# Kernel tuning notes

Measured on AMD Instinct MI355X. Metric: run time of the kernel, lower is better.

The kernel has to match this reference:

```python
import jax, jax.numpy as jnp
import numpy as np

EPS = 1e-8  # torch F.cosine_similarity norm clamp


def setup_inputs() -> dict:
    key = jax.random.key(0)
    ks = jax.random.split(key, 5)
    B, H, C, S, CS, K = 256, 256, 16384, 64, 32, 8
    query = jax.random.normal(ks[0], (B, H), dtype=jnp.float32)
    episode_embeddings = jax.random.normal(ks[1], (C, H), dtype=jnp.float32)
    episodes = jax.random.normal(ks[2], (C, S, H), dtype=jnp.float32)
    compressed_episodes = jax.random.normal(ks[3], (C, CS, H), dtype=jnp.float32)
    is_compressed = jax.random.randint(ks[4], (C,), 0, 2) == 1
    return {
        "query": query,
        "episode_embeddings": episode_embeddings,
        "episodes": episodes,
        "compressed_episodes": compressed_episodes,
        "is_compressed": is_compressed,
        "k": K,
    }


def reference(query, episode_embeddings, episodes, compressed_episodes, is_compressed, k):
    # cosine similarity  [B, C]
    qn = query / jnp.maximum(jnp.linalg.norm(query, axis=-1, keepdims=True), EPS)
    en = episode_embeddings / jnp.maximum(
        jnp.linalg.norm(episode_embeddings, axis=-1, keepdims=True), EPS)
    sim = qn @ en.T
    top_scores, top_idx = jax.lax.top_k(sim, k)  # [B, k]

    S = episodes.shape[1]
    CS = compressed_episodes.shape[1]
    full = episodes[top_idx]                # [B, k, S, H] gather
    comp = compressed_episodes[top_idx]     # [B, k, CS, H] gather
    comp_padded = jnp.pad(comp, ((0, 0), (0, 0), (0, S - CS), (0, 0)))
    flag = is_compressed[top_idx][..., None, None]  # [B, k, 1, 1]
    retrieved = jnp.where(flag, comp_padded, full)  # [B, k, S, H]
    return retrieved, top_scores
```

## Files before the change

### kernel.cpp

```cpp
#include <hip/hip_runtime.h>
#include <math.h>

#define B_  256
#define H_  256
#define C_  16384
#define S_  64
#define CS_ 32
#define K_  8
#define EPS 1e-8f
#define RET_ ((size_t)B_ * K_ * S_ * H_)

typedef __attribute__((ext_vector_type(8))) short short8v;
typedef __attribute__((ext_vector_type(4))) float f32x4;


__device__ inline unsigned short f2bf(float f) {
    unsigned u = __builtin_bit_cast(unsigned, f);
    unsigned r = u + 0x7fffu + ((u >> 16) & 1u);
    return (unsigned short)(r >> 16);
}
__device__ inline unsigned ordf(float f) {
    unsigned u = __builtin_bit_cast(unsigned, f);
    return u ^ ((u >> 31) ? 0xFFFFFFFFu : 0x80000000u);
}
__device__ inline short8v pack8(float4 a, float4 b) {
    short8v r;
    r[0] = (short)f2bf(a.x); r[1] = (short)f2bf(a.y);
    r[2] = (short)f2bf(a.z); r[3] = (short)f2bf(a.w);
    r[4] = (short)f2bf(b.x); r[5] = (short)f2bf(b.y);
    r[6] = (short)f2bf(b.z); r[7] = (short)f2bf(b.w);
    return r;
}
__device__ inline void ce(unsigned long long& a, unsigned long long& b) {
    unsigned long long lo = a < b ? a : b;
    a = a < b ? b : a;
    b = lo;
}
__device__ inline void merge_shfl(unsigned long long best[8], int xorlane) {
    unsigned long long m[8];
    #pragma unroll
    for (int i = 0; i < 8; ++i) {
        unsigned long long p = __shfl_xor(best[7 - i], xorlane);
        m[i] = best[i] > p ? best[i] : p;
    }
    ce(m[0], m[4]); ce(m[1], m[5]); ce(m[2], m[6]); ce(m[3], m[7]);
    ce(m[0], m[2]); ce(m[1], m[3]); ce(m[4], m[6]); ce(m[5], m[7]);
    ce(m[0], m[1]); ce(m[2], m[3]); ce(m[4], m[5]); ce(m[6], m[7]);
    #pragma unroll
    for (int i = 0; i < 8; ++i) best[i] = m[i];
}

#define LSTR 40
__global__ __launch_bounds__(256) void simsel_kernel(const float* __restrict__ q,
                                                     const float* __restrict__ e,
                                                     const unsigned* __restrict__ icw,
                                                     unsigned long long* __restrict__ candbuf,
                                                     int* __restrict__ mode) {
    const int t = threadIdx.x;
    if (blockIdx.x == 1024) {
        __shared__ int f;
        if (t == 0) f = 0;
        __syncthreads();
        int any = 0;
        for (int i = t; i < 4096; i += 256)
            if (icw[i] & 0xFFFFFF00u) any = 1;
        if (any) atomicOr(&f, 1);
        __syncthreads();
        if (t == 0) *mode = f;
        return;
    }

    __shared__ union {
        unsigned short st[4][64 * LSTR];
        float tile[64 * 65];
    } sm;
    __shared__ float einv_s[64];
    const int lane = t & 63, wv = t >> 6;
    const int wm = wv >> 1, wn = wv & 1;
    const int bid = blockIdx.x;
    const int ct = (bid & 7) * 32 + (bid >> 5);
    const int bt = (bid >> 3) & 3;
    const int c0 = ct * 64, b0 = bt * 64;
    const int r = t >> 2, g = t & 3;
    const float4* q4 = (const float4*)q;
    const float4* e4 = (const float4*)e;

    float esq = 0.f;
    f32x4 acc[2][2];
    #pragma unroll
    for (int i = 0; i < 2; ++i)
        #pragma unroll
        for (int j = 0; j < 2; ++j) acc[i][j] = (f32x4){0.f, 0.f, 0.f, 0.f};

    {
        float4 qa0 = q4[(size_t)(b0 + r) * 64 + g * 2];
        float4 qa1 = q4[(size_t)(b0 + r) * 64 + g * 2 + 1];
        float4 ea0 = e4[(size_t)(c0 + r) * 64 + g * 2];
        float4 ea1 = e4[(size_t)(c0 + r) * 64 + g * 2 + 1];
        esq += ea0.x * ea0.x + ea0.y * ea0.y + ea0.z * ea0.z + ea0.w * ea0.w
             + ea1.x * ea1.x + ea1.y * ea1.y + ea1.z * ea1.z + ea1.w * ea1.w;
        *(short8v*)&sm.st[0][r * LSTR + g * 8] = pack8(qa0, qa1);
        *(short8v*)&sm.st[2][r * LSTR + g * 8] = pack8(ea0, ea1);
    }

    for (int hc = 0; hc < 8; ++hc) {
        const int cur = hc & 1, nxt = cur ^ 1;
        float4 qa0, qa1, ea0, ea1;
        if (hc < 7) {
            qa0 = q4[(size_t)(b0 + r) * 64 + (hc + 1) * 8 + g * 2];
            qa1 = q4[(size_t)(b0 + r) * 64 + (hc + 1) * 8 + g * 2 + 1];
            ea0 = e4[(size_t)(c0 + r) * 64 + (hc + 1) * 8 + g * 2];
            ea1 = e4[(size_t)(c0 + r) * 64 + (hc + 1) * 8 + g * 2 + 1];
        }
        __syncthreads();

        short8v afr[2], bfr[2];
        #pragma unroll
        for (int mi = 0; mi < 2; ++mi)
            afr[mi] = *(short8v*)&sm.st[cur][(wm * 32 + mi * 16 + (lane & 15)) * LSTR + (lane >> 4) * 8];
        #pragma unroll
        for (int ni = 0; ni < 2; ++ni)
            bfr[ni] = *(short8v*)&sm.st[2 + cur][(wn * 32 + ni * 16 + (lane & 15)) * LSTR + (lane >> 4) * 8];
        #pragma unroll
        for (int mi = 0; mi < 2; ++mi)
            #pragma unroll
            for (int ni = 0; ni < 2; ++ni)
                acc[mi][ni] = __builtin_amdgcn_mfma_f32_16x16x32_bf16(
                    afr[mi], bfr[ni], acc[mi][ni], 0, 0, 0);

        if (hc < 7) {
            esq += ea0.x * ea0.x + ea0.y * ea0.y + ea0.z * ea0.z + ea0.w * ea0.w
                 + ea1.x * ea1.x + ea1.y * ea1.y + ea1.z * ea1.z + ea1.w * ea1.w;
            *(short8v*)&sm.st[nxt][r * LSTR + g * 8] = pack8(qa0, qa1);
            *(short8v*)&sm.st[2 + nxt][r * LSTR + g * 8] = pack8(ea0, ea1);
        }
    }

    esq += __shfl_xor(esq, 1);
    esq += __shfl_xor(esq, 2);
    if (g == 0) einv_s[r] = 1.0f / fmaxf(sqrtf(esq), EPS);
    __syncthreads();

    #pragma unroll
    for (int mi = 0; mi < 2; ++mi)
        #pragma unroll
        for (int j = 0; j < 4; ++j) {
            int row = wm * 32 + mi * 16 + (lane >> 4) * 4 + j;
            #pragma unroll
            for (int ni = 0; ni < 2; ++ni) {
                int col = wn * 32 + ni * 16 + (lane & 15);
                sm.tile[row * 65 + col] = acc[mi][ni][j] * einv_s[col];
            }
        }
    __syncthreads();

    unsigned long long best[8];
    #pragma unroll
    for (int k = 0; k < 8; ++k) best[k] = 0ull;
    for (int i = 0; i < 16; ++i) {
        int c = g * 16 + i;
        float v = sm.tile[r * 65 + c];
        unsigned long long key = ((unsigned long long)ordf(v) << 32)
                               | (unsigned)(0xFFFFFFFFu - (unsigned)(c0 + c));
        if (key > best[7]) {
            best[7] = key;
            #pragma unroll
            for (int k = 7; k > 0; --k)
                if (best[k] > best[k - 1]) {
                    unsigned long long tmp = best[k];
                    best[k] = best[k - 1]; best[k - 1] = tmp;
                }
        }
    }
    merge_shfl(best, 1);
    merge_shfl(best, 2);
    if (g == 0) {
        #pragma unroll
        for (int k = 0; k < 8; ++k)
            candbuf[(size_t)(b0 + r) * 2048 + ct * 8 + k] = best[k];
    }
}

__global__ __launch_bounds__(256) void merge_kernel(const float* __restrict__ q,
                                                    const float* __restrict__ e,
                                                    const unsigned long long* __restrict__ candbuf,
                                                    float* __restrict__ out_scores,
                                                    int* __restrict__ top_idx) {
    __shared__ unsigned long long wtop[4][32];
    __shared__ unsigned long long m2[2][32];
    __shared__ unsigned long long sel32[32];
    __shared__ float rs[32];
    __shared__ int   ri[32];
    const int t = threadIdx.x, b = blockIdx.x;
    const int wv = t >> 6, lane = t & 63;

    const unsigned long long* lp = candbuf + (size_t)b * 2048 + (size_t)(wv * 64 + lane) * 8;
    unsigned long long k0 = lp[0], k1 = lp[1], k2 = lp[2], k3 = lp[3],
                       k4 = lp[4], k5 = lp[5], k6 = lp[6], k7 = lp[7];
    int p = 0;
    unsigned long long cur = k0;

    for (int it = 0; it < 32; ++it) {
        unsigned long long km = cur;
        #pragma unroll
        for (int d = 1; d < 64; d <<= 1) {
            unsigned long long o = __shfl_xor(km, d);
            km = o > km ? o : km;
        }
        if (lane == 0) wtop[wv][it] = km;
        if (cur == km) {
            ++p;
            cur = (p == 1) ? k1 : (p == 2) ? k2 : (p == 3) ? k3 : (p == 4) ? k4
                : (p == 5) ? k5 : (p == 6) ? k6 : (p == 7) ? k7 : 0ull;
        }
    }
    __syncthreads();

    if (wv < 2) {
        unsigned long long v = (lane < 32) ? wtop[2 * wv][lane]
                                           : wtop[2 * wv + 1][63 - lane];
        #pragma unroll
        for (int d = 32; d > 0; d >>= 1) {
            unsigned long long o = __shfl_xor(v, d);
            v = ((lane & d) == 0) ? (v > o ? v : o) : (v < o ? v : o);
        }
        if (lane < 32) m2[wv][lane] = v;
    }
    __syncthreads();
    if (wv == 0) {
        unsigned long long v = (lane < 32) ? m2[0][lane] : m2[1][63 - lane];
        #pragma unroll
        for (int d = 32; d > 0; d >>= 1) {
            unsigned long long o = __shfl_xor(v, d);
            v = ((lane & d) == 0) ? (v > o ? v : o) : (v < o ? v : o);
        }
        if (lane < 32) sel32[lane] = v;
    }
    __syncthreads();

    float4 qv = ((const float4*)q)[(size_t)b * 64 + lane];
    float qsq = qv.x * qv.x + qv.y * qv.y + qv.z * qv.z + qv.w * qv.w;
    #pragma unroll
    for (int d = 1; d < 64; d <<= 1) qsq += __shfl_xor(qsq, d);
    float qi = 1.0f / fmaxf(sqrtf(qsq), EPS);

    for (int m = wv; m < 32; m += 4) {
        int idx = (int)(0xFFFFFFFFu - (unsigned)(sel32[m] & 0xFFFFFFFFull));
        float4 ev = ((const float4*)e)[(size_t)idx * 64 + lane];
        float dot = qv.x * ev.x + qv.y * ev.y + qv.z * ev.z + qv.w * ev.w;
        float ss  = ev.x * ev.x + ev.y * ev.y + ev.z * ev.z + ev.w * ev.w;
        #pragma unroll
        for (int d = 1; d < 64; d <<= 1) {
            dot += __shfl_xor(dot, d);
            ss  += __shfl_xor(ss, d);
        }
        if (lane == 0) {
            rs[m] = dot * qi * (1.0f / fmaxf(sqrtf(ss), EPS));
            ri[m] = idx;
        }
    }
    __syncthreads();

    if (t < 64) {
        float val; int idx, slot;
        if (t < 32) { val = rs[t]; idx = ri[t]; slot = t; }
        else        { val = -INFINITY; idx = 0x7fffffff; slot = -1; }
        for (int pp = 0; pp < 8; ++pp) {
            float bs = val; int bi = idx, bsl = slot;
            #pragma unroll
            for (int d = 1; d < 64; d <<= 1) {
                float os = __shfl_xor(bs, d);
                int   oi = __shfl_xor(bi, d);
                int   osl = __shfl_xor(bsl, d);
                if (os > bs || (os == bs && oi < bi)) { bs = os; bi = oi; bsl = osl; }
            }
            if (t == 0) { out_scores[b * K_ + pp] = bs; top_idx[b * K_ + pp] = bi; }
            if (slot == bsl) val = -INFINITY;
        }
    }
}

__global__ __launch_bounds__(256) void gather_kernel(const float* __restrict__ epi,
                                                     const float* __restrict__ comp,
                                                     const void* __restrict__ icp,
                                                     const int* __restrict__ top_idx,
                                                     const int* __restrict__ mode,
                                                     float* __restrict__ out) {
    const int bj = blockIdx.x;
    const int c = top_idx[bj];
    const int m = *mode;
    const int flag = m ? (((const unsigned char*)icp)[c] != 0)
                       : (((const int*)icp)[c] != 0);
    const int t = threadIdx.x;
    f32x4* o4 = (f32x4*)out + (size_t)bj * 4096;
    if (!flag) {
        const f32x4* s4 = (const f32x4*)epi + (size_t)c * 4096;
        #pragma unroll 4
        for (int i = t; i < 4096; i += 256)
            __builtin_nontemporal_store(__builtin_nontemporal_load(s4 + i), o4 + i);
    } else {
        const f32x4* s4 = (const f32x4*)comp + (size_t)c * 2048;
        #pragma unroll 4
        for (int i = t; i < 2048; i += 256)
            __builtin_nontemporal_store(__builtin_nontemporal_load(s4 + i), o4 + i);
        const f32x4 z = (f32x4){0.f, 0.f, 0.f, 0.f};
        #pragma unroll 4
        for (int i = 2048 + t; i < 4096; i += 256)
            __builtin_nontemporal_store(z, o4 + i);
    }
}

extern "C" void kernel_launch(void* const* d_in, const int* in_sizes, int n_in,
                              void* d_out, int out_size, void* d_ws, size_t ws_size,
                              hipStream_t stream) {
    const float* query = (const float*)d_in[0];
    const float* emb   = (const float*)d_in[1];
    const float* epi   = (const float*)d_in[2];
    const float* comp  = (const float*)d_in[3];
    const void*  icp   = d_in[4];
    float* out = (float*)d_out;

    unsigned long long* candbuf = (unsigned long long*)d_ws;
    int* mode   = (int*)((char*)d_ws + (4u << 20));
    int* topidx = mode + 1;
    float* out_scores = out + RET_;

    simsel_kernel<<<1025, 256, 0, stream>>>(query, emb, (const unsigned*)icp,
                                            candbuf, mode);
    merge_kernel<<<B_, 256, 0, stream>>>(query, emb, candbuf, out_scores, topidx);
    gather_kernel<<<B_ * K_, 256, 0, stream>>>(epi, comp, icp, topidx, mode, out);
}
```

Before: 104.0 us.

## Fuse three stages into one persistent cooperative kernel with grid syncs

The similarity/top-k, merge and gather kernels are merged into one cooperative persistent kernel. Each stage runs as a grid-stride loop and grid-wide barriers replace the kernel boundaries. This removes two launch gaps and drains. In exchange there is a grid sync cost, shared memory unioned across phases, fewer blocks than the original gather grid, and host-side occupancy queries on every call. The three separate kernels remain as a fallback if the cooperative launch fails.

```diff
diff --git a/kernel.cpp b/kernel.cpp
--- a/kernel.cpp
+++ b/kernel.cpp
@@ -1,5 +1,8 @@
 #include <hip/hip_runtime.h>
+#include <hip/hip_cooperative_groups.h>
 #include <math.h>
+
+namespace cg = cooperative_groups;
 
 #define B_  256
 #define H_  256
@@ -51,35 +54,27 @@
 }
 
 #define LSTR 40
-__global__ __launch_bounds__(256) void simsel_kernel(const float* __restrict__ q,
-                                                     const float* __restrict__ e,
-                                                     const unsigned* __restrict__ icw,
-                                                     unsigned long long* __restrict__ candbuf,
-                                                     int* __restrict__ mode) {
-    const int t = threadIdx.x;
-    if (blockIdx.x == 1024) {
-        __shared__ int f;
-        if (t == 0) f = 0;
-        __syncthreads();
-        int any = 0;
-        for (int i = t; i < 4096; i += 256)
-            if (icw[i] & 0xFFFFFF00u) any = 1;
-        if (any) atomicOr(&f, 1);
-        __syncthreads();
-        if (t == 0) *mode = f;
-        return;
-    }
-
-    __shared__ union {
-        unsigned short st[4][64 * LSTR];
-        float tile[64 * 65];
-    } sm;
-    __shared__ float einv_s[64];
+
+union SimselSM {
+    unsigned short st[4][64 * LSTR];
+    float tile[64 * 65];
+};
+struct MergeSM {
+    unsigned long long wtop[4][32];
+    unsigned long long m2[2][32];
+    unsigned long long sel32[32];
+    float rs[32];
+    int   ri[32];
+};
+
+__device__ inline void simsel_body(int tile, int t, SimselSM& sm, float* einv_s,
+                                   const float* __restrict__ q,
+                                   const float* __restrict__ e,
+                                   unsigned long long* __restrict__ candbuf) {
     const int lane = t & 63, wv = t >> 6;
     const int wm = wv >> 1, wn = wv & 1;
-    const int bid = blockIdx.x;
-    const int ct = (bid & 7) * 32 + (bid >> 5);
-    const int bt = (bid >> 3) & 3;
+    const int ct = (tile & 7) * 32 + (tile >> 5);
+    const int bt = (tile >> 3) & 3;
     const int c0 = ct * 64, b0 = bt * 64;
     const int r = t >> 2, g = t & 3;
     const float4* q4 = (const float4*)q;
@@ -181,19 +176,13 @@
     }
 }
 
-__global__ __launch_bounds__(256) void merge_kernel(const float* __restrict__ q,
-                                                    const float* __restrict__ e,
-                                                    const unsigned long long* __restrict__ candbuf,
-                                                    float* __restrict__ out_scores,
-                                                    int* __restrict__ top_idx) {
-    __shared__ unsigned long long wtop[4][32];
-    __shared__ unsigned long long m2[2][32];
-    __shared__ unsigned long long sel32[32];
-    __shared__ float rs[32];
-    __shared__ int   ri[32];
-    const int t = threadIdx.x, b = blockIdx.x;
+__device__ inline void merge_body(int b, int t, MergeSM& sm,
+                                  const float* __restrict__ q,
+                                  const float* __restrict__ e,
+                                  const unsigned long long* __restrict__ candbuf,
+                                  float* __restrict__ out_scores,
+                                  int* __restrict__ top_idx) {
     const int wv = t >> 6, lane = t & 63;
-
     const unsigned long long* lp = candbuf + (size_t)b * 2048 + (size_t)(wv * 64 + lane) * 8;
     unsigned long long k0 = lp[0], k1 = lp[1], k2 = lp[2], k3 = lp[3],
                        k4 = lp[4], k5 = lp[5], k6 = lp[6], k7 = lp[7];
@@ -207,7 +196,7 @@
             unsigned long long o = __shfl_xor(km, d);
             km = o > km ? o : km;
         }
-        if (lane == 0) wtop[wv][it] = km;
+        if (lane == 0) sm.wtop[wv][it] = km;
         if (cur == km) {
             ++p;
             cur = (p == 1) ? k1 : (p == 2) ? k2 : (p == 3) ? k3 : (p == 4) ? k4
@@ -217,24 +206,24 @@
     __syncthreads();
 
     if (wv < 2) {
-        unsigned long long v = (lane < 32) ? wtop[2 * wv][lane]
-                                           : wtop[2 * wv + 1][63 - lane];
+        unsigned long long v = (lane < 32) ? sm.wtop[2 * wv][lane]
+                                           : sm.wtop[2 * wv + 1][63 - lane];
         #pragma unroll
         for (int d = 32; d > 0; d >>= 1) {
             unsigned long long o = __shfl_xor(v, d);
             v = ((lane & d) == 0) ? (v > o ? v : o) : (v < o ? v : o);
         }
-        if (lane < 32) m2[wv][lane] = v;
+        if (lane < 32) sm.m2[wv][lane] = v;
     }
     __syncthreads();
     if (wv == 0) {
-        unsigned long long v = (lane < 32) ? m2[0][lane] : m2[1][63 - lane];
+        unsigned long long v = (lane < 32) ? sm.m2[0][lane] : sm.m2[1][63 - lane];
         #pragma unroll
         for (int d = 32; d > 0; d >>= 1) {
             unsigned long long o = __shfl_xor(v, d);
             v = ((lane & d) == 0) ? (v > o ? v : o) : (v < o ? v : o);
         }
-        if (lane < 32) sel32[lane] = v;
+        if (lane < 32) sm.sel32[lane] = v;
     }
     __syncthreads();
 
@@ -245,7 +234,7 @@
     float qi = 1.0f / fmaxf(sqrtf(qsq), EPS);
 
     for (int m = wv; m < 32; m += 4) {
-        int idx = (int)(0xFFFFFFFFu - (unsigned)(sel32[m] & 0xFFFFFFFFull));
+        int idx = (int)(0xFFFFFFFFu - (unsigned)(sm.sel32[m] & 0xFFFFFFFFull));
         float4 ev = ((const float4*)e)[(size_t)idx * 64 + lane];
         float dot = qv.x * ev.x + qv.y * ev.y + qv.z * ev.z + qv.w * ev.w;
         float ss  = ev.x * ev.x + ev.y * ev.y + ev.z * ev.z + ev.w * ev.w;
@@ -255,15 +244,15 @@
             ss  += __shfl_xor(ss, d);
         }
         if (lane == 0) {
-            rs[m] = dot * qi * (1.0f / fmaxf(sqrtf(ss), EPS));
-            ri[m] = idx;
+            sm.rs[m] = dot * qi * (1.0f / fmaxf(sqrtf(ss), EPS));
+            sm.ri[m] = idx;
         }
     }
     __syncthreads();
 
     if (t < 64) {
         float val; int idx, slot;
-        if (t < 32) { val = rs[t]; idx = ri[t]; slot = t; }
+        if (t < 32) { val = sm.rs[t]; idx = sm.ri[t]; slot = t; }
         else        { val = -INFINITY; idx = 0x7fffffff; slot = -1; }
         for (int pp = 0; pp < 8; ++pp) {
             float bs = val; int bi = idx, bsl = slot;
@@ -280,18 +269,27 @@
     }
 }
 
-__global__ __launch_bounds__(256) void gather_kernel(const float* __restrict__ epi,
-                                                     const float* __restrict__ comp,
-                                                     const void* __restrict__ icp,
-                                                     const int* __restrict__ top_idx,
-                                                     const int* __restrict__ mode,
-                                                     float* __restrict__ out) {
-    const int bj = blockIdx.x;
+__device__ inline void detect_body(int t, const unsigned* __restrict__ icw,
+                                   int* __restrict__ mode, int* fsh) {
+    if (t == 0) *fsh = 0;
+    __syncthreads();
+    int any = 0;
+    for (int i = t; i < 4096; i += 256)
+        if (icw[i] & 0xFFFFFF00u) any = 1;
+    if (any) atomicOr(fsh, 1);
+    __syncthreads();
+    if (t == 0) *mode = *fsh;
+}
+
+__device__ inline void gather_body(int bj, int t, int m_,
+                                   const float* __restrict__ epi,
+                                   const float* __restrict__ comp,
+                                   const void* __restrict__ icp,
+                                   const int* __restrict__ top_idx,
+                                   float* __restrict__ out) {
     const int c = top_idx[bj];
-    const int m = *mode;
-    const int flag = m ? (((const unsigned char*)icp)[c] != 0)
-                       : (((const int*)icp)[c] != 0);
-    const int t = threadIdx.x;
+    const int flag = m_ ? (((const unsigned char*)icp)[c] != 0)
+                        : (((const int*)icp)[c] != 0);
     f32x4* o4 = (f32x4*)out + (size_t)bj * 4096;
     if (!flag) {
         const f32x4* s4 = (const f32x4*)epi + (size_t)c * 4096;
@@ -310,6 +308,66 @@
     }
 }
 
+__global__ __launch_bounds__(256) void fused_kernel(
+        const float* __restrict__ q, const float* __restrict__ e,
+        const float* __restrict__ epi, const float* __restrict__ comp,
+        const void* __restrict__ icp,
+        unsigned long long* __restrict__ candbuf,
+        int* __restrict__ mode, int* __restrict__ top_idx,
+        float* __restrict__ out, float* __restrict__ out_scores,
+        int grid) {
+    __shared__ union { SimselSM p1; MergeSM p2; } sm;
+    __shared__ float einv_s[64];
+    __shared__ int fsh;
+    const int t = threadIdx.x, bid = blockIdx.x;
+
+    for (int tile = bid; tile < 1024; tile += grid) {
+        __syncthreads();
+        simsel_body(tile, t, sm.p1, einv_s, q, e, candbuf);
+    }
+    cg::this_grid().sync();
+
+    for (int b = bid; b < 257; b += grid) {
+        __syncthreads();
+        if (b < 256) merge_body(b, t, sm.p2, q, e, candbuf, out_scores, top_idx);
+        else         detect_body(t, (const unsigned*)icp, mode, &fsh);
+    }
+    cg::this_grid().sync();
+
+    const int m_ = *mode;
+    for (int bj = bid; bj < 2048; bj += grid)
+        gather_body(bj, t, m_, epi, comp, icp, top_idx, out);
+}
+
+__global__ __launch_bounds__(256) void simsel_kernel(const float* __restrict__ q,
+                                                     const float* __restrict__ e,
+                                                     const unsigned* __restrict__ icw,
+                                                     unsigned long long* __restrict__ candbuf,
+                                                     int* __restrict__ mode) {
+    __shared__ union { SimselSM p1; } sm;
+    __shared__ float einv_s[64];
+    __shared__ int fsh;
+    const int t = threadIdx.x;
+    if (blockIdx.x == 1024) { detect_body(t, icw, mode, &fsh); return; }
+    simsel_body(blockIdx.x, t, sm.p1, einv_s, q, e, candbuf);
+}
+__global__ __launch_bounds__(256) void merge_kernel(const float* __restrict__ q,
+                                                    const float* __restrict__ e,
+                                                    const unsigned long long* __restrict__ candbuf,
+                                                    float* __restrict__ out_scores,
+                                                    int* __restrict__ top_idx) {
+    __shared__ MergeSM sm;
+    merge_body(blockIdx.x, threadIdx.x, sm, q, e, candbuf, out_scores, top_idx);
+}
+__global__ __launch_bounds__(256) void gather_kernel(const float* __restrict__ epi,
+                                                     const float* __restrict__ comp,
+                                                     const void* __restrict__ icp,
+                                                     const int* __restrict__ top_idx,
+                                                     const int* __restrict__ mode,
+                                                     float* __restrict__ out) {
+    gather_body(blockIdx.x, threadIdx.x, *mode, epi, comp, icp, top_idx, out);
+}
+
 extern "C" void kernel_launch(void* const* d_in, const int* in_sizes, int n_in,
                               void* d_out, int out_size, void* d_ws, size_t ws_size,
                               hipStream_t stream) {
@@ -325,8 +383,27 @@
     int* topidx = mode + 1;
     float* out_scores = out + RET_;
 
-    simsel_kernel<<<1025, 256, 0, stream>>>(query, emb, (const unsigned*)icp,
-                                            candbuf, mode);
-    merge_kernel<<<B_, 256, 0, stream>>>(query, emb, candbuf, out_scores, topidx);
-    gather_kernel<<<B_ * K_, 256, 0, stream>>>(epi, comp, icp, topidx, mode, out);
-}
+    int dev = 0;
+    hipGetDevice(&dev);
+    int numCU = 0;
+    hipDeviceGetAttribute(&numCU, hipDeviceAttributeMultiprocessorCount, dev);
+    int perCU = 0;
+    hipOccupancyMaxActiveBlocksPerMultiprocessor(&perCU, fused_kernel, 256, 0);
+
+    bool ok = false;
+    if (numCU > 0 && perCU > 0) {
+        int grid = numCU * perCU;
+        if (grid > 1024) grid = 1024;
+        void* args[] = { (void*)&query, (void*)&emb, (void*)&epi, (void*)&comp,
+                         (void*)&icp, (void*)&candbuf, (void*)&mode, (void*)&topidx,
+                         (void*)&out, (void*)&out_scores, (void*)&grid };
+        ok = (hipLaunchCooperativeKernel((const void*)fused_kernel, dim3(grid),
+                                         dim3(256), args, 0, stream) == hipSuccess);
+    }
+    if (!ok) {
+        simsel_kernel<<<1025, 256, 0, stream>>>(query, emb, (const unsigned*)icp,
+                                                candbuf, mode);
+        merge_kernel<<<B_, 256, 0, stream>>>(query, emb, candbuf, out_scores, topidx);
+        gather_kernel<<<B_ * K_, 256, 0, stream>>>(epi, comp, icp, topidx, mode, out);
+    }
+}
```

New measurement: 191.5 us. +84.1%, slower.
